# Optimization experiments

Hardware: AMD Instinct MI355X
Metric: run time of the kernel (lower is better)

Reference implementation:

```python
import jax, jax.numpy as jnp
import numpy as np

B, C, H, W = 16, 256, 56, 56
HEADS = 4
C_OUT = 256
K = 3
SQ = 16  # squeeze_rate (C=256 >= 80, so not halved)
BN_EPS = 1e-5


def setup_inputs() -> dict:
    key = jax.random.key(0)
    ks = jax.random.split(key, 9)
    r = C // SQ
    cper = C_OUT // HEADS
    return {
        "x": jax.random.normal(ks[0], (B, C, H, W), dtype=jnp.float32),
        "bn_gamma": 1.0 + 0.1 * jax.random.normal(ks[1], (C,), dtype=jnp.float32),
        "bn_beta": 0.1 * jax.random.normal(ks[2], (C,), dtype=jnp.float32),
        "bn_mean": 0.1 * jax.random.normal(ks[3], (C,), dtype=jnp.float32),
        "bn_var": 0.5 + jax.random.uniform(ks[4], (C,), dtype=jnp.float32),
        "fc1_w": 0.1 * jax.random.normal(ks[5], (HEADS, r, C), dtype=jnp.float32),
        "fc2_w": 0.1 * jax.random.normal(ks[6], (HEADS, C, r), dtype=jnp.float32),
        "fc2_b": jnp.ones((HEADS, C), dtype=jnp.float32),  # init.constant_(bias, 1.0)
        "conv_w": 0.05 * jax.random.normal(ks[7], (HEADS, cper, C, K, K), dtype=jnp.float32),
        "inactive_channels": 192,
    }


def reference(x, bn_gamma, bn_beta, bn_mean, bn_var, fc1_w, fc2_w, fc2_b, conv_w, inactive_channels):
    b, c, h, w = x.shape
    heads = fc1_w.shape[0]
    # BatchNorm (inference, running stats) + ReLU
    inv = jax.lax.rsqrt(bn_var + BN_EPS)
    xn = jax.nn.relu((x - bn_mean[None, :, None, None]) * (bn_gamma * inv)[None, :, None, None]
                     + bn_beta[None, :, None, None])
    # Global average pool -> [b, c]
    x_avg = xn.mean(axis=(2, 3))
    # Per-head SE gate: relu(fc2(relu(fc1(x_avg))))  -> [heads, b, c]
    y1 = jax.nn.relu(jnp.einsum("bc,hrc->hbr", x_avg, fc1_w))
    mask = jax.nn.relu(jnp.einsum("hbr,hcr->hbc", y1, fc2_w) + fc2_b[:, None, :])
    lasso_loss = mask.mean(axis=(1, 2)).sum()  # sum over heads of per-head mean
    # topk smallest -> threshold; zero out mask values <= k-th smallest (detached cmp)
    mask_d = jax.lax.stop_gradient(mask)
    if inactive_channels > 0:
        neg_vals, _ = jax.lax.top_k(-mask_d, inactive_channels)  # k largest of -mask
        thresh = -neg_vals[..., -1:]  # k-th smallest of mask, [heads, b, 1]
        mask_c = jnp.where(mask_d <= thresh, 0.0, mask)
    else:
        mask_c = mask
    # Apply per-head channel mask and stack heads: [b, heads*c, h, w]
    mc = jnp.transpose(mask_c, (1, 0, 2))  # [b, heads, c]
    x_mask = (xn[:, None, :, :, :] * mc[:, :, :, None, None]).reshape(b, heads * c, h, w)
    # Grouped conv (groups=heads), weight [heads*cper, c, K, K]
    wflat = conv_w.reshape(-1, c, K, K)
    out = jax.lax.conv_general_dilated(
        x_mask, wflat, window_strides=(1, 1), padding=[(1, 1), (1, 1)],
        dimension_numbers=("NCHW", "OIHW", "NCHW"), feature_group_count=heads)
    bo, co, ho, wo = out.shape
    out = out.reshape(bo, heads, co // heads, ho, wo).transpose(0, 2, 1, 3, 4).reshape(bo, co, ho, wo)
    return out, lasso_loss
```

## Files before the change

kernel.cpp:

```cpp
#include <hip/hip_runtime.h>
#include <hip/hip_bf16.h>
#include <math.h>

#define B_     16
#define C_     256
#define H_     56
#define W_     56
#define HEADS_ 4
#define CPER_  64
#define R_     16
#define HW_    (H_*W_)
#define BN_EPS_ 1e-5f

typedef short bf16x8 __attribute__((ext_vector_type(8)));
typedef float f32x4  __attribute__((ext_vector_type(4)));

__device__ inline unsigned short f2bf(float f) {
    unsigned int u = __builtin_bit_cast(unsigned int, f);
    u += 0x7fffu + ((u >> 16) & 1u);
    return (unsigned short)(u >> 16);
}

__global__ __launch_bounds__(64) void k_pool(
    const float* __restrict__ x,
    const float* __restrict__ gamma, const float* __restrict__ beta,
    const float* __restrict__ mean,  const float* __restrict__ var,
    float* __restrict__ xavg)
{
    int plane = blockIdx.x;
    int c = plane & (C_ - 1);
    float s = gamma[c] * rsqrtf(var[c] + BN_EPS_);
    float t = fmaf(-mean[c], s, beta[c]);
    const float4* xp = (const float4*)(x + (size_t)plane * HW_);
    float sum = 0.f;
    for (int i = threadIdx.x; i < HW_ / 4; i += 64) {
        float4 v = xp[i];
        sum += fmaxf(fmaf(v.x, s, t), 0.f) + fmaxf(fmaf(v.y, s, t), 0.f)
             + fmaxf(fmaf(v.z, s, t), 0.f) + fmaxf(fmaf(v.w, s, t), 0.f);
    }
    for (int off = 32; off; off >>= 1) sum += __shfl_down(sum, off, 64);
    if (threadIdx.x == 0) xavg[plane] = sum * (1.f / HW_);
}

__global__ __launch_bounds__(256) void k_se(
    const float* __restrict__ xavg,
    const float* __restrict__ fc1, const float* __restrict__ fc2,
    const float* __restrict__ fc2b, const int* __restrict__ kptr,
    float* __restrict__ maskc, int* __restrict__ aidx64,
    int* __restrict__ act_cnt, float* __restrict__ lasso)
{
    int hb = blockIdx.x;
    int h = hb / B_, b = hb - h * B_;
    int tid = threadIdx.x;

    __shared__ float sav[C_], sy1[R_], smask[C_], sred[4], sthr;
    __shared__ int scnt, s_ord[C_];

    sav[tid] = xavg[b * C_ + tid];
    if (tid == 0) scnt = 0;
    __syncthreads();

    if (tid < R_) {
        const float* w = fc1 + (size_t)(h * R_ + tid) * C_;
        float acc = 0.f;
        for (int c2 = 0; c2 < C_; ++c2) acc = fmaf(sav[c2], w[c2], acc);
        sy1[tid] = fmaxf(acc, 0.f);
    }
    __syncthreads();

    const float* w2 = fc2 + (size_t)(h * C_ + tid) * R_;
    float acc = fc2b[h * C_ + tid];
    for (int r = 0; r < R_; ++r) acc = fmaf(sy1[r], w2[r], acc);
    float m = fmaxf(acc, 0.f);
    smask[tid] = m;
    __syncthreads();

    float ls = m;
    for (int off = 32; off > 0; off >>= 1) ls += __shfl_down(ls, off, 64);
    int lane = tid & 63, wv = tid >> 6;
    if (lane == 0) sred[wv] = ls;

    int cl = 0, ce = 0;
    for (int j = 0; j < C_; ++j) {
        float vj = smask[j];
        cl += (vj < m);
        ce += (vj == m);
    }
    if (tid == 0) sthr = -1e30f;
    __syncthreads();
    int k = kptr[0];
    if (k > 0 && cl <= k - 1 && (k - 1) < cl + ce) sthr = m;
    __syncthreads();

    float thr = sthr;
    float mc = (m <= thr) ? 0.f : m;
    maskc[hb * C_ + tid] = mc;
    if (mc != 0.f) {
        int p = atomicAdd(&scnt, 1);
        s_ord[p] = tid;
    }
    __syncthreads();
    if (tid < 64) aidx64[hb * 64 + tid] = (tid < scnt) ? s_ord[tid] : 0;
    if (tid == 0) {
        act_cnt[hb] = scnt;
        atomicAdd(lasso, (sred[0] + sred[1] + sred[2] + sred[3]) * (1.f / (B_ * C_)));
    }
}

__global__ __launch_bounds__(256) void k_wgather(
    const float* __restrict__ convw, const float* __restrict__ maskc,
    const int* __restrict__ aidx64, const int* __restrict__ acnt,
    short* __restrict__ Wc)
{
    int t = blockIdx.x, hb = blockIdx.y;
    int h = hb >> 4;
    int tid = threadIdx.x;
    int cnt = acnt[hb];
    __shared__ int s_act[64];
    __shared__ float s_mv[64];
    if (tid < 64) {
        int a = aidx64[hb * 64 + tid];
        s_act[tid] = a;
        s_mv[tid]  = (tid < cnt) ? maskc[hb * C_ + a] : 0.f;
    }
    __syncthreads();
    const float* wsrc = convw + (size_t)h * CPER_ * C_ * 9;
    short* wdst = Wc + (size_t)(hb * 9 + t) * (CPER_ * 64);
    for (int it = 0; it < 16; ++it) {
        int e = it * 256 + tid;
        int cp = e & 63, j = e >> 6;
        float v = wsrc[((size_t)j * C_ + s_act[cp]) * 9 + t] * s_mv[cp];
        int slot = (cp + 8 * (j & 7)) & 63;
        wdst[j * 64 + slot] = (short)f2bf(v);
    }
}

__global__ __launch_bounds__(256) void k_bnc(
    const float* __restrict__ x,
    const float* __restrict__ gamma, const float* __restrict__ beta,
    const float* __restrict__ mean,  const float* __restrict__ var,
    const int* __restrict__ aidx64, short* __restrict__ xc)
{
    int y = blockIdx.x, b = blockIdx.y;
    int tid = threadIdx.x;
    int h = tid >> 6;
    __shared__ __align__(16) unsigned short T[W_ * 256];

    int c = aidx64[(h * B_ + b) * 64 + (tid & 63)];
    float s = gamma[c] * rsqrtf(var[c] + BN_EPS_);
    float t0 = fmaf(-mean[c], s, beta[c]);
    const float* xrow = x + ((size_t)(b * C_ + c)) * HW_ + y * W_;
    #pragma unroll
    for (int f = 0; f < 14; ++f) {
        float4 v = *(const float4*)(xrow + f * 4);
        int px = f * 4;
        T[(px + 0) * 256 + tid] = f2bf(fmaxf(fmaf(v.x, s, t0), 0.f));
        T[(px + 1) * 256 + tid] = f2bf(fmaxf(fmaf(v.y, s, t0), 0.f));
        T[(px + 2) * 256 + tid] = f2bf(fmaxf(fmaf(v.z, s, t0), 0.f));
        T[(px + 3) * 256 + tid] = f2bf(fmaxf(fmaf(v.w, s, t0), 0.f));
    }
    __syncthreads();

    const uint2* Ts = (const uint2*)T;
    uint2* ob = (uint2*)xc;
    #pragma unroll
    for (int it = 0; it < 14; ++it) {
        int e = it * 256 + tid;
        int px = e >> 6, col4 = e & 63;
        int hh = col4 >> 4, cp4 = col4 & 15;
        uint2 v = Ts[px * 64 + col4];
        ob[((size_t)(hh * B_ + b) * HW_ + (size_t)y * W_ + px) * 16 + cp4] = v;
    }
}

__global__ __launch_bounds__(256, 2) void k_conv(
    const short* __restrict__ xc, const short* __restrict__ Wc,
    float* __restrict__ out)
{
    int g = blockIdx.x;
    int vx = g & 7, r = g >> 3;
    int hb = vx * 8 + r / 14;
    int band = r - (r / 14) * 14;
    int h = hb >> 4, b = hb & 15;
    int tid = threadIdx.x, lane = tid & 63, wv = tid >> 6;
    int m = lane & 15, q = lane >> 4;
    int yrow = band * 4 + wv;

    __shared__ short sW[9 * 4096];

    const short* Wh = Wc + (size_t)hb * 9 * 4096;
    const short* xb = xc + (size_t)hb * HW_ * 64;

    #pragma unroll
    for (int it = 0; it < 18; ++it) {
        int e = it * 256 + tid;
        *(bf16x8*)&sW[e * 8] = *(const bf16x8*)(Wh + e * 8);
    }
    __syncthreads();

    f32x4 acc[4][4];
    #pragma unroll
    for (int i = 0; i < 4; ++i)
        #pragma unroll
        for (int j = 0; j < 4; ++j)
            #pragma unroll
            for (int rr = 0; rr < 4; ++rr) acc[i][j][rr] = 0.f;

    int arot = q * 8 + 8 * (m & 7);

    #pragma unroll
    for (int t = 0; t < 9; ++t) {
        const int dy = t / 3 - 1, dx = t % 3 - 1;
        int gy = yrow + dy;
        bool gyok = (unsigned)gy < (unsigned)H_;
        const short* sWc = sW + t * 4096;

        #pragma unroll
        for (int c0 = 0; c0 < 64; c0 += 32) {
            bf16x8 aF[4], bF[4];
            #pragma unroll
            for (int jt = 0; jt < 4; ++jt)
                aF[jt] = *(const bf16x8*)&sWc[(jt * 16 + m) * 64 + ((c0 + arot) & 63)];
            #pragma unroll
            for (int xt = 0; xt < 4; ++xt) {
                int gx = xt * 16 + m + dx;
                bf16x8 v = {0, 0, 0, 0, 0, 0, 0, 0};
                if (gyok && (unsigned)gx < (unsigned)W_)
                    v = *(const bf16x8*)(xb + ((size_t)(gy * W_ + gx)) * 64 + c0 + q * 8);
                bF[xt] = v;
            }
            #pragma unroll
            for (int jt = 0; jt < 4; ++jt)
                #pragma unroll
                for (int xt = 0; xt < 4; ++xt)
                    acc[jt][xt] = __builtin_amdgcn_mfma_f32_16x16x32_bf16(
                        aF[jt], bF[xt], acc[jt][xt], 0, 0, 0);
        }
    }

    #pragma unroll
    for (int xt = 0; xt < 4; ++xt) {
        int xx = xt * 16 + m;
        if (xx < W_) {
            #pragma unroll
            for (int jt = 0; jt < 4; ++jt)
                #pragma unroll
                for (int rr = 0; rr < 4; ++rr) {
                    int j = jt * 16 + q * 4 + rr;
                    int oc = j * HEADS_ + h;
                    out[(((size_t)b * C_ + oc) * H_ + yrow) * W_ + xx] = acc[jt][xt][rr];
                }
        }
    }
}

extern "C" void kernel_launch(void* const* d_in, const int* in_sizes, int n_in,
                              void* d_out, int out_size, void* d_ws, size_t ws_size,
                              hipStream_t stream)
{
    const float* x     = (const float*)d_in[0];
    const float* gamma = (const float*)d_in[1];
    const float* beta  = (const float*)d_in[2];
    const float* mean  = (const float*)d_in[3];
    const float* var   = (const float*)d_in[4];
    const float* fc1   = (const float*)d_in[5];
    const float* fc2   = (const float*)d_in[6];
    const float* fc2b  = (const float*)d_in[7];
    const float* convw = (const float*)d_in[8];
    const int*   kptr  = (const int*)d_in[9];

    float* out   = (float*)d_out;
    float* lasso = out + (size_t)B_ * C_ * HW_;

    char* ws = (char*)d_ws;
    size_t off = 0;
    short* xc    = (short*)(ws + off); off += (size_t)HEADS_ * B_ * HW_ * 64 * 2;
    off = (off + 255) & ~(size_t)255;
    float* xavg  = (float*)(ws + off); off += (size_t)B_ * C_ * 4;
    float* maskc = (float*)(ws + off); off += (size_t)HEADS_ * B_ * C_ * 4;
    int*   aidx64= (int*)  (ws + off); off += (size_t)HEADS_ * B_ * 64 * 4;
    int*   acnt  = (int*)  (ws + off); off += (size_t)HEADS_ * B_ * 4;
    off = (off + 255) & ~(size_t)255;
    short* Wc    = (short*)(ws + off); off += (size_t)HEADS_ * B_ * 9 * CPER_ * 64 * 2;

    hipMemsetAsync(lasso, 0, 4, stream);

    k_pool<<<B_ * C_, 64, 0, stream>>>(x, gamma, beta, mean, var, xavg);
    k_se<<<HEADS_ * B_, 256, 0, stream>>>(xavg, fc1, fc2, fc2b, kptr,
                                          maskc, aidx64, acnt, lasso);
    k_wgather<<<dim3(9, HEADS_ * B_), 256, 0, stream>>>(convw, maskc, aidx64, acnt, Wc);
    k_bnc<<<dim3(H_, B_), 256, 0, stream>>>(x, gamma, beta, mean, var, aidx64, xc);
    k_conv<<<HEADS_ * B_ * (H_ / 4), 256, 0, stream>>>(xc, Wc, out);
}
```

Baseline: 190.6 us.

## Software-pipeline conv operand loads and pack four planes per pool block

The conv kernel's 9-tap by 2-chunk loop is flattened into 18 steps. Global activation fragments are prefetched two steps ahead into a triple buffer, and LDS weight fragments one step ahead into a double buffer, so load latency overlaps the MFMA work. The first two activation loads are issued before the weight staging into LDS, which hides them behind that copy. The pooling kernel now handles four planes per 256-thread block instead of one plane per 64-thread block, cutting block count and launch overhead; the extra buffers raise register pressure, which could lower occupancy under the existing launch bounds.

Measured after the change: 192.3 us. About the same (+0.8%).

```diff
diff --git a/kernel.cpp b/kernel.cpp
--- a/kernel.cpp
+++ b/kernel.cpp
@@ -21,25 +21,26 @@
     return (unsigned short)(u >> 16);
 }
 
-__global__ __launch_bounds__(64) void k_pool(
+__global__ __launch_bounds__(256) void k_pool(
     const float* __restrict__ x,
     const float* __restrict__ gamma, const float* __restrict__ beta,
     const float* __restrict__ mean,  const float* __restrict__ var,
     float* __restrict__ xavg)
 {
-    int plane = blockIdx.x;
+    int wv = threadIdx.x >> 6, ln = threadIdx.x & 63;
+    int plane = blockIdx.x * 4 + wv;
     int c = plane & (C_ - 1);
     float s = gamma[c] * rsqrtf(var[c] + BN_EPS_);
     float t = fmaf(-mean[c], s, beta[c]);
     const float4* xp = (const float4*)(x + (size_t)plane * HW_);
     float sum = 0.f;
-    for (int i = threadIdx.x; i < HW_ / 4; i += 64) {
+    for (int i = ln; i < HW_ / 4; i += 64) {
         float4 v = xp[i];
         sum += fmaxf(fmaf(v.x, s, t), 0.f) + fmaxf(fmaf(v.y, s, t), 0.f)
              + fmaxf(fmaf(v.z, s, t), 0.f) + fmaxf(fmaf(v.w, s, t), 0.f);
     }
     for (int off = 32; off; off >>= 1) sum += __shfl_down(sum, off, 64);
-    if (threadIdx.x == 0) xavg[plane] = sum * (1.f / HW_);
+    if (ln == 0) xavg[plane] = sum * (1.f / HW_);
 }
 
 __global__ __launch_bounds__(256) void k_se(
@@ -185,11 +186,40 @@
     int tid = threadIdx.x, lane = tid & 63, wv = tid >> 6;
     int m = lane & 15, q = lane >> 4;
     int yrow = band * 4 + wv;
+    int arot = q * 8 + 8 * (m & 7);
 
     __shared__ short sW[9 * 4096];
 
     const short* Wh = Wc + (size_t)hb * 9 * 4096;
-    const short* xb = xc + (size_t)hb * HW_ * 64;
+    const short* xb = xc + (size_t)hb * HW_ * 64 + q * 8;
+
+    bf16x8 bFb[3][4];
+    bf16x8 aFb[2][4];
+
+#define LOADB_(kk) { \
+        const int t_ = (kk) >> 1, c0_ = ((kk) & 1) * 32; \
+        const int dy_ = t_ / 3 - 1, dx_ = t_ % 3 - 1; \
+        int gy_ = yrow + dy_; \
+        bool ok_ = (unsigned)gy_ < (unsigned)H_; \
+        _Pragma("unroll") \
+        for (int xt_ = 0; xt_ < 4; ++xt_) { \
+            int gx_ = xt_ * 16 + m + dx_; \
+            bf16x8 v_ = {0, 0, 0, 0, 0, 0, 0, 0}; \
+            if (ok_ && (unsigned)gx_ < (unsigned)W_) \
+                v_ = *(const bf16x8*)(xb + ((size_t)(gy_ * W_ + gx_)) * 64 + c0_); \
+            bFb[(kk) % 3][xt_] = v_; \
+        } }
+
+#define LOADA_(kk) { \
+        const int t_ = (kk) >> 1, c0_ = ((kk) & 1) * 32; \
+        const short* sWc_ = sW + t_ * 4096; \
+        _Pragma("unroll") \
+        for (int jt_ = 0; jt_ < 4; ++jt_) \
+            aFb[(kk) % 2][jt_] = *(const bf16x8*)&sWc_[(jt_ * 16 + m) * 64 + ((c0_ + arot) & 63)]; \
+        }
+
+    LOADB_(0);
+    LOADB_(1);
 
     #pragma unroll
     for (int it = 0; it < 18; ++it) {
@@ -206,37 +236,21 @@
             #pragma unroll
             for (int rr = 0; rr < 4; ++rr) acc[i][j][rr] = 0.f;
 
-    int arot = q * 8 + 8 * (m & 7);
-
-    #pragma unroll
-    for (int t = 0; t < 9; ++t) {
-        const int dy = t / 3 - 1, dx = t % 3 - 1;
-        int gy = yrow + dy;
-        bool gyok = (unsigned)gy < (unsigned)H_;
-        const short* sWc = sW + t * 4096;
-
+    LOADA_(0);
+
+    #pragma unroll
+    for (int k = 0; k < 18; ++k) {
+        if (k + 2 < 18) LOADB_(k + 2);
+        if (k + 1 < 18) LOADA_(k + 1);
         #pragma unroll
-        for (int c0 = 0; c0 < 64; c0 += 32) {
-            bf16x8 aF[4], bF[4];
+        for (int jt = 0; jt < 4; ++jt)
             #pragma unroll
-            for (int jt = 0; jt < 4; ++jt)
-                aF[jt] = *(const bf16x8*)&sWc[(jt * 16 + m) * 64 + ((c0 + arot) & 63)];
-            #pragma unroll
-            for (int xt = 0; xt < 4; ++xt) {
-                int gx = xt * 16 + m + dx;
-                bf16x8 v = {0, 0, 0, 0, 0, 0, 0, 0};
-                if (gyok && (unsigned)gx < (unsigned)W_)
-                    v = *(const bf16x8*)(xb + ((size_t)(gy * W_ + gx)) * 64 + c0 + q * 8);
-                bF[xt] = v;
-            }
-            #pragma unroll
-            for (int jt = 0; jt < 4; ++jt)
-                #pragma unroll
-                for (int xt = 0; xt < 4; ++xt)
-                    acc[jt][xt] = __builtin_amdgcn_mfma_f32_16x16x32_bf16(
-                        aF[jt], bF[xt], acc[jt][xt], 0, 0, 0);
-        }
-    }
+            for (int xt = 0; xt < 4; ++xt)
+                acc[jt][xt] = __builtin_amdgcn_mfma_f32_16x16x32_bf16(
+                    aFb[k % 2][jt], bFb[k % 3][xt], acc[jt][xt], 0, 0, 0);
+    }
+#undef LOADB_
+#undef LOADA_
 
     #pragma unroll
     for (int xt = 0; xt < 4; ++xt) {
@@ -285,7 +299,7 @@
 
     hipMemsetAsync(lasso, 0, 4, stream);
 
-    k_pool<<<B_ * C_, 64, 0, stream>>>(x, gamma, beta, mean, var, xavg);
+    k_pool<<<B_ * C_ / 4, 256, 0, stream>>>(x, gamma, beta, mean, var, xavg);
     k_se<<<HEADS_ * B_, 256, 0, stream>>>(xavg, fc1, fc2, fc2b, kptr,
                                           maskc, aidx64, acnt, lasso);
     k_wgather<<<dim3(9, HEADS_ * B_), 256, 0, stream>>>(convw, maskc, aidx64, acnt, Wc);
```
